# Optimization experiments

Hardware: AMD Instinct MI355X
Metric: run time of the kernel (lower is better)

Reference implementation:

```python
import jax, jax.numpy as jnp
import numpy as np

V, D, S, B, NL = 32000, 512, 1024, 2, 2
DS, KC, DI, DFF, E, TOPK = 16, 4, 1024, 2048, 8, 2
EPS = 1e-6


def rmsnorm(x, w):
    return x * jax.lax.rsqrt(jnp.mean(x * x, -1, keepdims=True) + EPS) * w


def mamba(x, in_w, conv_w, conv_b, x_proj_w, dt_w, dt_b, A_log, out_w):
    # x: (B, S, D)
    Bb, L, _ = x.shape
    xz = x @ in_w.T                      # (B, S, 2*DI)
    xi, z = jnp.split(xz, 2, axis=-1)    # each (B, S, DI)
    # causal depthwise conv (pad k-1 left == torch pad k-1 both + trim to L)
    xc = jnp.swapaxes(xi, 1, 2)          # (B, DI, S)
    xc = jax.lax.conv_general_dilated(
        xc, conv_w, window_strides=(1,), padding=[(KC - 1, 0)],
        dimension_numbers=("NCH", "OIH", "NCH"), feature_group_count=DI)
    xi = jnp.swapaxes(xc + conv_b[None, :, None], 1, 2)  # (B, S, DI)
    x_dbl = xi @ x_proj_w.T              # (B, S, 2*DS)
    B_param = x_dbl[..., DS:]            # (B, S, DS); first chunk overwritten in source
    delta = jax.nn.softplus(xi @ dt_w.T + dt_b)          # (B, S, DS)
    A = -jnp.exp(A_log)                  # (DI, DS)
    # recurrence coefficients (state dim summed out, as in source)
    a = jnp.exp(delta[:, :, None, :] * A[None, None]).sum(-1)        # (B, S, DI)
    b = xi * (delta * B_param).sum(-1, keepdims=True)                # (B, S, DI)

    def step(y, ab):
        at, bt = ab
        y = at * y + bt
        return y, y

    _, ys = jax.lax.scan(step, jnp.zeros((Bb, DI), x.dtype),
                         (jnp.swapaxes(a, 0, 1), jnp.swapaxes(b, 0, 1)))
    y = jnp.swapaxes(ys, 0, 1)           # (B, S, DI)
    y = y * jax.nn.silu(z)
    return y @ out_w.T                   # (B, S, D)


def moe(x, rw, rb, w1, b1, w2, b2):
    router_logits = x @ rw.T + rb                     # (B, S, E)
    probs = jax.nn.softmax(router_logits, axis=-1)
    topv, topi = jax.lax.top_k(probs, TOPK)
    wts = topv / topv.sum(-1, keepdims=True)          # renormalized gates
    h = jax.nn.gelu(jnp.einsum("bsd,efd->bsef", x, w1) + b1)   # (B, S, E, DFF)
    eo = jnp.einsum("bsef,edf->bsed", h, w2) + b2               # (B, S, E, D)
    sel = jnp.take_along_axis(eo, topi[..., None], axis=2)      # (B, S, K, D)
    out = (wts[..., None] * sel).sum(2)
    # load-balancing aux loss
    f = jax.nn.one_hot(topi, E).sum(2).mean((0, 1)) / TOPK
    P = probs.mean((0, 1))
    aux = E * jnp.sum(f * P)
    return out, aux


def setup_inputs() -> dict:
    key = jax.random.key(0)
    ks = jax.random.split(key, 16)
    f = lambda k, s: jax.random.normal(k, s, dtype=jnp.float32) * 0.02
    return {
        "input_ids": jax.random.randint(ks[0], (B, S), 0, V),
        "tok_emb": f(ks[1], (V, D)),
        "pos_emb": f(ks[2], (S, D)),
        "norm1_w": jnp.ones((NL, D), jnp.float32),
        "norm2_w": jnp.ones((NL, D), jnp.float32),
        "in_proj_w": f(ks[3], (NL, 2 * DI, D)),
        "conv_w": f(ks[4], (NL, DI, 1, KC)),
        "conv_b": jnp.zeros((NL, DI), jnp.float32),
        "x_proj_w": f(ks[5], (NL, 2 * DS, DI)),
        "dt_proj_w": f(ks[6], (NL, DS, DI)),
        "dt_proj_b": jnp.zeros((NL, DS), jnp.float32),
        "A_log": jnp.tile(jnp.log(jnp.arange(1, DS + 1, dtype=jnp.float32)), (NL, DI, 1)),
        "D_param": jnp.ones((NL, DI), jnp.float32),  # unused in forward, as in source
        "out_proj_w": f(ks[7], (NL, D, DI)),
        "router_w": f(ks[8], (NL, E, D)),
        "router_b": jnp.zeros((NL, E), jnp.float32),
        "w1": f(ks[9], (NL, E, DFF, D)),
        "b1": jnp.zeros((NL, E, DFF), jnp.float32),
        "w2": f(ks[10], (NL, E, D, DFF)),
        "b2": jnp.zeros((NL, E, D), jnp.float32),
        "final_norm_w": jnp.ones((D,), jnp.float32),
        "lm_head_w": f(ks[11], (V, D)),
    }


def reference(input_ids, tok_emb, pos_emb, norm1_w, norm2_w, in_proj_w, conv_w,
              conv_b, x_proj_w, dt_proj_w, dt_proj_b, A_log, D_param, out_proj_w,
              router_w, router_b, w1, b1, w2, b2, final_norm_w, lm_head_w):
    x = tok_emb[input_ids] + pos_emb[None, :, :]
    aux_total = jnp.zeros((), x.dtype)
    for l in range(NL):
        m = mamba(rmsnorm(x, norm1_w[l]), in_proj_w[l], conv_w[l], conv_b[l],
                  x_proj_w[l], dt_proj_w[l], dt_proj_b[l], A_log[l], out_proj_w[l])
        x = x + m
        ff, aux = moe(rmsnorm(x, norm2_w[l]), router_w[l], router_b[l],
                      w1[l], b1[l], w2[l], b2[l])
        x = x + ff
        aux_total = aux_total + aux
    x = rmsnorm(x, final_norm_w)
    logits = x @ lm_head_w.T
    return logits, aux_total
```

## Files before the change

kernel.cpp:

```cpp
#include <hip/hip_runtime.h>
#include <math.h>

#define S_    1024
#define D_    512
#define DI_   1024
#define DS_   16
#define KC_   4
#define E_    8
#define DFF_  2048
#define NTOK  2048
#define VOCAB 32000
#define NCHUNK 16
#define CHL    64
#define NSLOT 4096

typedef unsigned short ushort;
typedef unsigned int   uint;
typedef __attribute__((ext_vector_type(8))) short short8;
typedef __attribute__((ext_vector_type(4))) float f32x4;

#define IN_US   0ull
#define INL_US  1048576ull
#define OUT_US  2097152ull
#define OUTL_US 2621440ull
#define W1_US   3145728ull
#define W1L_US  11534336ull
#define W2_US   19922944ull
#define W2L_US  28311552ull
#define LAYER_US 36700160ull
#define LM_US   73400320ull
#define IN4   262144
#define OUT4  393216
#define W14   2490368
#define L4    4587520
#define LM4   4096000
#define LMEND 13271040
#define TOT4  13279232

__device__ __forceinline__ float gelu_sig(float x){
  float u = x*(1.5957691216057308f + 0.07135481627f*x*x);
  return x / (1.0f + expf(-u));
}
__device__ __forceinline__ ushort f2bf_rnd(float f){
  uint u = __float_as_uint(f);
  return (ushort)((u + 0x8000u) >> 16);
}
__device__ __forceinline__ float bf2f(ushort h){
  return __uint_as_float(((uint)h) << 16);
}
__device__ __forceinline__ void split1(float f, ushort& h, ushort& l){
  h = f2bf_rnd(f);
  float fh = bf2f(h);
  l = (ushort)(__float_as_uint(f - fh) >> 16);
}
__device__ __forceinline__ void gl16(void* lds, const void* g){
  __builtin_amdgcn_global_load_lds(
      (const __attribute__((address_space(1))) void*)g,
      (__attribute__((address_space(3))) void*)lds, 16, 0, 0);
}

__global__ __launch_bounds__(128) void k_embed(const int* __restrict__ ids,
    const float* __restrict__ tok, const float* __restrict__ pos, float* __restrict__ x){
  int t  = blockIdx.x;
  int d4 = threadIdx.x << 2;
  int s  = t & (S_-1);
  int id = ids[t];
  float4 tv = *(const float4*)(tok + (size_t)id*D_ + d4);
  float4 pv = *(const float4*)(pos + (size_t)s*D_ + d4);
  float4 o; o.x=tv.x+pv.x; o.y=tv.y+pv.y; o.z=tv.z+pv.z; o.w=tv.w+pv.w;
  *(float4*)(x + (size_t)t*D_ + d4) = o;
}

__global__ __launch_bounds__(256) void k_split_all(
    const float* __restrict__ in_w, const float* __restrict__ out_w,
    const float* __restrict__ w1, const float* __restrict__ w2,
    const float* __restrict__ lm, const float* __restrict__ Alog,
    ushort* __restrict__ wsp, float* __restrict__ negA){
  int g = blockIdx.x*256 + threadIdx.x;
  if (g >= TOT4) return;
  if (g < 2*L4){
    int l = (g < L4) ? 0 : 1;
    int r = g - l*L4;
    const float* src; size_t dh_off, dl_off;
    if (r < IN4){
      src = in_w + (size_t)l*1048576 + (size_t)r*4;
      dh_off = (size_t)l*LAYER_US + IN_US  + (size_t)r*4;
      dl_off = (size_t)l*LAYER_US + INL_US + (size_t)r*4;
    } else if (r < OUT4){
      int r2 = r - IN4;
      src = out_w + (size_t)l*524288 + (size_t)r2*4;
      dh_off = (size_t)l*LAYER_US + OUT_US  + (size_t)r2*4;
      dl_off = (size_t)l*LAYER_US + OUTL_US + (size_t)r2*4;
    } else if (r < W14){
      int r3 = r - OUT4;
      src = w1 + (size_t)l*8388608 + (size_t)r3*4;
      dh_off = (size_t)l*LAYER_US + W1_US  + (size_t)r3*4;
      dl_off = (size_t)l*LAYER_US + W1L_US + (size_t)r3*4;
    } else {
      int r4 = r - W14;
      src = w2 + (size_t)l*8388608 + (size_t)r4*4;
      dh_off = (size_t)l*LAYER_US + W2_US  + (size_t)r4*4;
      dl_off = (size_t)l*LAYER_US + W2L_US + (size_t)r4*4;
    }
    float4 v = *(const float4*)src;
    ushort h0,h1,h2,h3,l0,l1,l2,l3;
    split1(v.x,h0,l0); split1(v.y,h1,l1); split1(v.z,h2,l2); split1(v.w,h3,l3);
    *(uint2*)(wsp + dh_off) = make_uint2((uint)h0|((uint)h1<<16), (uint)h2|((uint)h3<<16));
    *(uint2*)(wsp + dl_off) = make_uint2((uint)l0|((uint)l1<<16), (uint)l2|((uint)l3<<16));
  } else if (g < LMEND){
    int r = g - 2*L4;
    float4 v = *(const float4*)(lm + (size_t)r*4);
    ushort h0 = f2bf_rnd(v.x), h1 = f2bf_rnd(v.y), h2 = f2bf_rnd(v.z), h3 = f2bf_rnd(v.w);
    *(uint2*)(wsp + LM_US + (size_t)r*4) = make_uint2((uint)h0|((uint)h1<<16), (uint)h2|((uint)h3<<16));
  } else {
    int r = g - LMEND;
    float4 v = *(const float4*)(Alog + (size_t)r*4);
    float4 o; o.x=-expf(v.x); o.y=-expf(v.y); o.z=-expf(v.z); o.w=-expf(v.w);
    *(float4*)(negA + (size_t)r*4) = o;
  }
}

template<int ADD>
__global__ __launch_bounds__(128) void k_rmsnorm_split(float* __restrict__ x,
    const float* __restrict__ P3, const int* __restrict__ slotmap,
    const float* __restrict__ w, ushort* __restrict__ oh, ushort* __restrict__ ol){
  int t = blockIdx.x;
  int d4 = threadIdx.x << 2;
  float4 v = *(const float4*)(x + (size_t)t*D_ + d4);
  if (ADD){
    int s0 = slotmap[2*t], s1 = slotmap[2*t+1];
    #pragma unroll
    for (int ks=0; ks<4; ++ks){
      float4 p0 = *(const float4*)(P3 + ((size_t)ks*NSLOT + s0)*D_ + d4);
      float4 p1 = *(const float4*)(P3 + ((size_t)ks*NSLOT + s1)*D_ + d4);
      v.x += p0.x + p1.x; v.y += p0.y + p1.y; v.z += p0.z + p1.z; v.w += p0.w + p1.w;
    }
    *(float4*)(x + (size_t)t*D_ + d4) = v;
  }
  float ss = v.x*v.x + v.y*v.y + v.z*v.z + v.w*v.w;
  #pragma unroll
  for (int off=32; off>=1; off>>=1) ss += __shfl_down(ss, off);
  __shared__ float sred[2];
  if ((threadIdx.x & 63) == 0) sred[threadIdx.x >> 6] = ss;
  __syncthreads();
  float total = sred[0] + sred[1];
  float scale = 1.0f / sqrtf(total * (1.0f/D_) + 1e-6f);
  float4 wv = *(const float4*)(w + d4);
  float4 o; o.x=v.x*scale*wv.x; o.y=v.y*scale*wv.y; o.z=v.z*scale*wv.z; o.w=v.w*scale*wv.w;
  ushort h0,h1,h2,h3,l0,l1,l2,l3;
  split1(o.x,h0,l0); split1(o.y,h1,l1); split1(o.z,h2,l2); split1(o.w,h3,l3);
  *(uint2*)(oh + (size_t)t*D_ + d4) = make_uint2((uint)h0|((uint)h1<<16), (uint)h2|((uint)h3<<16));
  *(uint2*)(ol + (size_t)t*D_ + d4) = make_uint2((uint)l0|((uint)l1<<16), (uint)l2|((uint)l3<<16));
}

__global__ __launch_bounds__(128) void k_rmsnorm_router(float* __restrict__ x,
    const float* __restrict__ P2, const float* __restrict__ w,
    const float* __restrict__ rw, const float* __restrict__ rb,
    ushort* __restrict__ oh, ushort* __restrict__ ol,
    float* __restrict__ probs, float* __restrict__ topw, int* __restrict__ topi){
  int t = blockIdx.x;
  int tid = threadIdx.x;
  int d4 = tid << 2;
  float4 v = *(const float4*)(x + (size_t)t*D_ + d4);
  #pragma unroll
  for (int ks=0; ks<4; ++ks){
    float4 p = *(const float4*)(P2 + (size_t)ks*NTOK*D_ + (size_t)t*D_ + d4);
    v.x += p.x; v.y += p.y; v.z += p.z; v.w += p.w;
  }
  *(float4*)(x + (size_t)t*D_ + d4) = v;
  float ss = v.x*v.x + v.y*v.y + v.z*v.z + v.w*v.w;
  #pragma unroll
  for (int off=32; off>=1; off>>=1) ss += __shfl_down(ss, off);
  __shared__ float sred[2];
  __shared__ float lg2[2][E_];
  __shared__ float lg[E_];
  if ((tid & 63) == 0) sred[tid >> 6] = ss;
  __syncthreads();
  float total = sred[0] + sred[1];
  float scale = 1.0f / sqrtf(total * (1.0f/D_) + 1e-6f);
  float4 wv = *(const float4*)(w + d4);
  float4 o; o.x=v.x*scale*wv.x; o.y=v.y*scale*wv.y; o.z=v.z*scale*wv.z; o.w=v.w*scale*wv.w;
  ushort h0,h1,h2,h3,l0,l1,l2,l3;
  split1(o.x,h0,l0); split1(o.y,h1,l1); split1(o.z,h2,l2); split1(o.w,h3,l3);
  *(uint2*)(oh + (size_t)t*D_ + d4) = make_uint2((uint)h0|((uint)h1<<16), (uint)h2|((uint)h3<<16));
  *(uint2*)(ol + (size_t)t*D_ + d4) = make_uint2((uint)l0|((uint)l1<<16), (uint)l2|((uint)l3<<16));
  int lane = tid & 63, wid2 = tid >> 6;
  #pragma unroll
  for (int e=0;e<E_;e++){
    const float* rr = rw + (size_t)e*D_ + d4;
    float p = o.x*rr[0] + o.y*rr[1] + o.z*rr[2] + o.w*rr[3];
    #pragma unroll
    for (int off=32; off>=1; off>>=1) p += __shfl_down(p, off);
    if (lane==0) lg2[wid2][e] = p;
  }
  __syncthreads();
  if (tid==0){
    #pragma unroll
    for (int e=0;e<E_;e++) lg[e] = lg2[0][e] + lg2[1][e] + rb[e];
    float mx = lg[0];
    #pragma unroll
    for (int e=1;e<E_;e++) mx = fmaxf(mx, lg[e]);
    float pe[E_]; float sum = 0.f;
    #pragma unroll
    for (int e=0;e<E_;e++){ pe[e] = expf(lg[e]-mx); sum += pe[e]; }
    #pragma unroll
    for (int e=0;e<E_;e++){ pe[e] /= sum; probs[(size_t)t*E_ + e] = pe[e]; }
    int i1 = 0;
    #pragma unroll
    for (int e=1;e<E_;e++) if (pe[e] > pe[i1]) i1 = e;
    int i2 = (i1==0) ? 1 : 0;
    #pragma unroll
    for (int e=0;e<E_;e++) if (e!=i1 && pe[e] > pe[i2]) i2 = e;
    float wsum = pe[i1] + pe[i2];
    topw[t*2]   = pe[i1]/wsum;
    topw[t*2+1] = pe[i2]/wsum;
    topi[t*2] = i1; topi[t*2+1] = i2;
  }
}

template<int EPI, int NT, int KSP>
__global__ __launch_bounds__(256, 4) void gemm_mfma(
    const ushort* __restrict__ Ahg, const ushort* __restrict__ Alg,
    const ushort* __restrict__ Whb, const ushort* __restrict__ Wlb,
    float* __restrict__ Cb, ushort* __restrict__ Chh, ushort* __restrict__ Chl,
    const float* __restrict__ biasb, const float* __restrict__ slotw,
    const int* __restrict__ gidx, const int* __restrict__ offs,
    int M, int N, int K)
{
  int e, ksp;
  if (KSP > 1){ e = blockIdx.z / KSP; ksp = blockIdx.z % KSP; }
  else        { e = blockIdx.z;       ksp = 0; }
  int off = 0, cnt = M;
  if (EPI==1 || EPI==3){
    off = offs[e];
    cnt = offs[e+1] - off;
    if ((int)(blockIdx.x*128) >= cnt) return;
  }
  const size_t wbase = (size_t)((EPI==1||EPI==3) ? e : 0) * N * K;
  const ushort* Whg = Whb + wbase;
  const ushort* Wlg = Wlb + wbase;
  const float* bias = (EPI==1||EPI==3) ? (biasb + (size_t)e * N) : biasb;

  __shared__ ushort sAh[128*32];
  __shared__ ushort sWh[128*32];
  __shared__ ushort sAl[(NT>1)?(128*32):8];
  __shared__ ushort sWl[(NT>1)?(128*32):8];

  const int tid  = threadIdx.x;
  const int row0 = blockIdx.x * 128;
  const int col0 = blockIdx.y * 128;
  const int lane = tid & 63;
  const int wid  = tid >> 6;

  const int srow0  = wid*32 + (lane>>2);
  const int srow1  = srow0 + 16;
  const int schunk = (lane&3) ^ ((lane>>2)&3);
  const int ldsb0  = (wid*32)      * 32;
  const int ldsb1  = (wid*32 + 16) * 32;

  const int k0 = ksp * (K / KSP);
  const int nk = K / KSP;

  int ar0, ar1;
  if (EPI==1){
    int l0i = row0 + srow0; if (l0i > cnt-1) l0i = cnt-1;
    int l1i = row0 + srow1; if (l1i > cnt-1) l1i = cnt-1;
    ar0 = gidx[off + l0i]; ar1 = gidx[off + l1i];
  } else if (EPI==3){
    int l0i = row0 + srow0; if (l0i > cnt-1) l0i = cnt-1;
    int l1i = row0 + srow1; if (l1i > cnt-1) l1i = cnt-1;
    ar0 = off + l0i; ar1 = off + l1i;
  } else {
    ar0 = row0 + srow0; ar1 = row0 + srow1;
  }
  const ushort* gah0 = Ahg + (size_t)ar0*K + k0 + schunk*8;
  const ushort* gah1 = Ahg + (size_t)ar1*K + k0 + schunk*8;
  const ushort* gwh0 = Whg + (size_t)(col0 + srow0)*K + k0 + schunk*8;
  const ushort* gwh1 = Whg + (size_t)(col0 + srow1)*K + k0 + schunk*8;
  const ushort* gal0 = nullptr; const ushort* gal1 = nullptr;
  const ushort* gwl0 = nullptr; const ushort* gwl1 = nullptr;
  if (NT>1){
    gal0 = Alg + (size_t)ar0*K + k0 + schunk*8;
    gal1 = Alg + (size_t)ar1*K + k0 + schunk*8;
    gwl0 = Wlg + (size_t)(col0 + srow0)*K + k0 + schunk*8;
    gwl1 = Wlg + (size_t)(col0 + srow1)*K + k0 + schunk*8;
  }

  const int lr  = lane & 15;
  const int kq  = lane >> 4;
  const int kx  = ((kq ^ (lr & 3)) << 3);
  const int wrM = (wid >> 1) * 64;
  const int wcN = (wid & 1) * 64;

  f32x4 zero = {0.f, 0.f, 0.f, 0.f};
  f32x4 acc[4][4];
  #pragma unroll
  for (int i=0;i<4;i++)
    #pragma unroll
    for (int j=0;j<4;j++) acc[i][j] = zero;

  for (int kk=0; kk<nk; kk+=32){
    __syncthreads();
    gl16(&sAh[ldsb0], gah0 + kk);
    gl16(&sAh[ldsb1], gah1 + kk);
    gl16(&sWh[ldsb0], gwh0 + kk);
    gl16(&sWh[ldsb1], gwh1 + kk);
    if (NT>1){
      gl16(&sAl[ldsb0], gal0 + kk);
      gl16(&sAl[ldsb1], gal1 + kk);
      gl16(&sWl[ldsb0], gwl0 + kk);
      gl16(&sWl[ldsb1], gwl1 + kk);
    }
    __syncthreads();

    short8 fah[4], fal[4], fbh[4], fbl[4];
    #pragma unroll
    for (int f=0; f<4; ++f){
      int rA = wrM + f*16 + lr;
      int rB = wcN + f*16 + lr;
      fah[f] = *(const short8*)&sAh[rA*32 + kx];
      fbh[f] = *(const short8*)&sWh[rB*32 + kx];
      if (NT>1){
        fal[f] = *(const short8*)&sAl[rA*32 + kx];
        fbl[f] = *(const short8*)&sWl[rB*32 + kx];
      }
    }
    #pragma unroll
    for (int i=0;i<4;i++)
      #pragma unroll
      for (int j=0;j<4;j++){
        f32x4 c = acc[i][j];
        if (NT==4) c = __builtin_amdgcn_mfma_f32_16x16x32_bf16(fal[i], fbl[j], c, 0,0,0);
        if (NT>1){
          c = __builtin_amdgcn_mfma_f32_16x16x32_bf16(fal[i], fbh[j], c, 0,0,0);
          c = __builtin_amdgcn_mfma_f32_16x16x32_bf16(fah[i], fbl[j], c, 0,0,0);
        }
        c = __builtin_amdgcn_mfma_f32_16x16x32_bf16(fah[i], fbh[j], c, 0,0,0);
        acc[i][j] = c;
      }
  }

  float bj[4];
  if (EPI==1 || EPI==3){
    #pragma unroll
    for (int j=0;j<4;j++) bj[j] = bias[col0 + wcN + j*16 + lr];
  }
  #pragma unroll
  for (int i=0;i<4;i++){
    #pragma unroll
    for (int jj=0;jj<4;jj++){
      int rt   = wrM + i*16 + kq*4 + jj;
      int grow = row0 + rt;
      if (EPI==0){
        float* cr = Cb + (size_t)grow*N + col0 + wcN + lr;
        #pragma unroll
        for (int j=0;j<4;j++) cr[j*16] = acc[i][j][jj];
      } else if (EPI==2){
        float* cr = Cb + (size_t)ksp*M*N + (size_t)grow*N + col0 + wcN + lr;
        #pragma unroll
        for (int j=0;j<4;j++) cr[j*16] = acc[i][j][jj];
      } else if (EPI==1){
        if (grow < cnt){
          int slot = off + grow;
          size_t base = (size_t)slot*N + col0 + wcN + lr;
          #pragma unroll
          for (int j=0;j<4;j++){
            float g = gelu_sig(acc[i][j][jj] + bj[j]);
            ushort hh, ll; split1(g, hh, ll);
            Chh[base + j*16] = hh; Chl[base + j*16] = ll;
          }
        }
      } else {
        if (grow < cnt){
          int slot = off + grow;
          float sw = slotw[slot];
          float* cr = Cb + ((size_t)ksp*NSLOT + slot)*N + col0 + wcN + lr;
          #pragma unroll
          for (int j=0;j<4;j++){
            float v = acc[i][j][jj];
            if (ksp==0) v += bj[j];
            cr[j*16] = sw*v;
          }
        }
      }
    }
  }
}

__global__ __launch_bounds__(256) void k_convab(const float* __restrict__ xz,
    const float* __restrict__ cw, const float* __restrict__ cb,
    const float* __restrict__ xpw, const float* __restrict__ dtw,
    const float* __restrict__ dtb, const float* __restrict__ negA,
    float* __restrict__ a, float* __restrict__ bb){
  int t = blockIdx.x;
  int b = t >> 10, s = t & (S_-1);
  int tid = threadIdx.x;
  int c0 = tid << 2;
  __shared__ float xrow[DI_];
  __shared__ float outv[32];
  __shared__ float dl[DS_+1];
  float4 acc = *(const float4*)(cb + c0);
  #pragma unroll
  for (int k=0;k<KC_;k++){
    int ss = s - (KC_-1) + k;
    if (ss >= 0){
      float4 xv = *(const float4*)(xz + ((size_t)(b*S_+ss))*(2*DI_) + c0);
      acc.x += xv.x * cw[(c0+0)*KC_ + k];
      acc.y += xv.y * cw[(c0+1)*KC_ + k];
      acc.z += xv.z * cw[(c0+2)*KC_ + k];
      acc.w += xv.w * cw[(c0+3)*KC_ + k];
    }
  }
  *(float4*)(xrow + c0) = acc;
  __syncthreads();
  int wid = tid >> 6, lane = tid & 63;
  #pragma unroll
  for (int oi=0; oi<8; ++oi){
    int o = wid*8 + oi;
    const float* wr = (o < 16) ? (xpw + (size_t)(DS_ + o)*DI_) : (dtw + (size_t)(o-16)*DI_);
    float sum = 0.f;
    #pragma unroll
    for (int j=0;j<16;j++) sum += xrow[lane + 64*j] * wr[lane + 64*j];
    #pragma unroll
    for (int off=32; off>=1; off>>=1) sum += __shfl_down(sum, off);
    if (lane == 0) outv[o] = sum;
  }
  __syncthreads();
  if (tid < DS_){
    float d  = outv[16+tid] + dtb[tid];
    float sp = fmaxf(d, 0.f) + log1pf(expf(-fabsf(d)));
    dl[tid] = sp;
    float pr = sp * outv[tid];
    #pragma unroll
    for (int off=8; off>=1; off>>=1) pr += __shfl_down(pr, off);
    if (tid == 0) dl[DS_] = pr;
  }
  __syncthreads();
  float sdbv = dl[DS_];
  float av[4];
  #pragma unroll
  for (int i=0;i<4;i++){
    const float* nA = negA + (size_t)(c0+i)*DS_;
    float sum = 0.f;
    #pragma unroll
    for (int ds=0; ds<DS_; ds++) sum += expf(dl[ds] * nA[ds]);
    av[i] = sum;
  }
  *(float4*)(a + (size_t)t*DI_ + c0) = make_float4(av[0],av[1],av[2],av[3]);
  float4 bv; bv.x=acc.x*sdbv; bv.y=acc.y*sdbv; bv.z=acc.z*sdbv; bv.w=acc.w*sdbv;
  *(float4*)(bb + (size_t)t*DI_ + c0) = bv;
}

__global__ __launch_bounds__(256) void k_scan1(const float* __restrict__ a,
    const float* __restrict__ bb, float* __restrict__ aprod, float* __restrict__ yend){
  int g  = blockIdx.x*256 + threadIdx.x;
  int di = g & (DI_-1);
  int c  = (g >> 10) & (NCHUNK-1);
  int b  = g >> 14;
  float ap = 1.f, y = 0.f;
  size_t base = ((size_t)b*S_ + (size_t)c*CHL)*DI_ + di;
  #pragma unroll 4
  for (int i=0;i<CHL;i++){
    float at = a[base + (size_t)i*DI_], bt = bb[base + (size_t)i*DI_];
    y = at*y + bt; ap *= at;
  }
  aprod[g] = ap; yend[g] = y;
}

__global__ __launch_bounds__(256) void k_scan2(const float* __restrict__ a,
    const float* __restrict__ bb, const float* __restrict__ xz,
    const float* __restrict__ aprod, const float* __restrict__ yend,
    ushort* __restrict__ yh, ushort* __restrict__ yl){
  int g  = blockIdx.x*256 + threadIdx.x;
  int di = g & (DI_-1);
  int c  = (g >> 10) & (NCHUNK-1);
  int b  = g >> 14;
  float y = 0.f;
  for (int j=0;j<c;j++){
    int gg = ((b*NCHUNK + j) << 10) + di;
    y = aprod[gg]*y + yend[gg];
  }
  size_t base = ((size_t)b*S_ + (size_t)c*CHL)*DI_ + di;
  #pragma unroll 4
  for (int i=0;i<CHL;i++){
    float at = a[base + (size_t)i*DI_], bt = bb[base + (size_t)i*DI_];
    y = at*y + bt;
    float z = xz[((size_t)(b*S_ + c*CHL + i))*(2*DI_) + DI_ + di];
    float sil = z / (1.f + expf(-z));
    float v = y * sil;
    ushort hh, ll; split1(v, hh, ll);
    yh[base + (size_t)i*DI_] = hh;
    yl[base + (size_t)i*DI_] = ll;
  }
}

__global__ __launch_bounds__(512) void k_compact_aux(const int* __restrict__ topi,
    const float* __restrict__ topw, const float* __restrict__ probs,
    int* __restrict__ gidx, float* __restrict__ asgw, int* __restrict__ slotmap,
    int* __restrict__ offs, float* __restrict__ dst, int first){
  int tid = threadIdx.x;
  int e = tid >> 6, lane = tid & 63;
  __shared__ unsigned char stop[NTOK*2];
  __shared__ float stw[NTOK*2];
  __shared__ int counts[E_];
  __shared__ float red[8][E_];
  for (int i = tid; i < NTOK*2; i += 512){
    stop[i] = (unsigned char)topi[i];
    stw[i]  = topw[i];
  }
  float ps[E_];
  #pragma unroll
  for (int q=0;q<E_;q++) ps[q]=0.f;
  for (int t = tid; t < NTOK; t += 512){
    float4 p0 = *(const float4*)(probs + (size_t)t*E_);
    float4 p1 = *(const float4*)(probs + (size_t)t*E_ + 4);
    ps[0]+=p0.x; ps[1]+=p0.y; ps[2]+=p0.z; ps[3]+=p0.w;
    ps[4]+=p1.x; ps[5]+=p1.y; ps[6]+=p1.z; ps[7]+=p1.w;
  }
  #pragma unroll
  for (int q=0;q<E_;q++){
    float v = ps[q];
    #pragma unroll
    for (int off=32; off>=1; off>>=1) v += __shfl_down(v, off);
    if (lane==0) red[e][q] = v;
  }
  __syncthreads();
  int cnt = 0;
  for (int c=0; c<NTOK/64; ++c){
    int t = c*64 + lane;
    bool flag = (stop[2*t]==e) || (stop[2*t+1]==e);
    unsigned long long m = __ballot(flag);
    cnt += __popcll(m);
  }
  if (lane==0) counts[e] = cnt;
  __syncthreads();
  int base = 0;
  for (int i=0;i<e;i++) base += counts[i];
  if (lane==0) offs[e] = base;
  if (tid==0){
    int tot=0;
    for (int i=0;i<E_;i++) tot += counts[i];
    offs[E_] = tot;
  }
  int run = base;
  for (int c=0; c<NTOK/64; ++c){
    int t = c*64 + lane;
    int which = (stop[2*t]==e) ? 0 : ((stop[2*t+1]==e) ? 1 : -1);
    bool flag = which >= 0;
    unsigned long long m = __ballot(flag);
    int rank = __popcll(m & ((1ull<<lane)-1ull));
    if (flag){
      int pos = run + rank;
      gidx[pos] = t;
      asgw[pos] = stw[2*t+which];
      slotmap[2*t+which] = pos;
    }
    run += __popcll(m);
  }
  if (tid==0){
    float aux = 0.f;
    #pragma unroll
    for (int i=0;i<E_;i++){
      float P = 0.f;
      #pragma unroll
      for (int wdd=0; wdd<8; ++wdd) P += red[wdd][i];
      P *= (1.0f/NTOK);
      float f = (float)counts[i] * (1.0f/(NTOK*2.0f));
      aux += f*P;
    }
    aux *= (float)E_;
    if (first) dst[0] = aux; else dst[0] += aux;
  }
}

extern "C" void kernel_launch(void* const* d_in, const int* in_sizes, int n_in,
                              void* d_out, int out_size, void* d_ws, size_t ws_size,
                              hipStream_t stream) {
  const int*   input_ids  = (const int*)  d_in[0];
  const float* tok_emb    = (const float*)d_in[1];
  const float* pos_emb    = (const float*)d_in[2];
  const float* norm1_w    = (const float*)d_in[3];
  const float* norm2_w    = (const float*)d_in[4];
  const float* in_proj_w  = (const float*)d_in[5];
  const float* conv_w     = (const float*)d_in[6];
  const float* conv_b     = (const float*)d_in[7];
  const float* x_proj_w   = (const float*)d_in[8];
  const float* dt_proj_w  = (const float*)d_in[9];
  const float* dt_proj_b  = (const float*)d_in[10];
  const float* A_log      = (const float*)d_in[11];
  const float* out_proj_w = (const float*)d_in[13];
  const float* router_w   = (const float*)d_in[14];
  const float* router_b   = (const float*)d_in[15];
  const float* w1         = (const float*)d_in[16];
  const float* b1         = (const float*)d_in[17];
  const float* w2         = (const float*)d_in[18];
  const float* b2         = (const float*)d_in[19];
  const float* final_norm = (const float*)d_in[20];
  const float* lm_head_w  = (const float*)d_in[21];
  float* out = (float*)d_out;

  float* f0 = (float*)d_ws;
  float*  x    = f0;
  ushort* xnh  = (ushort*)(f0 + 1048576);
  ushort* xnl  = xnh + 1048576;
  float*  xz   = f0 + 2097152;
  float*  a    = f0 + 6291456;
  float*  bb   = f0 + 8388608;
  ushort* yh   = (ushort*)(f0 + 10485760);
  ushort* yl   = yh + 2097152;
  ushort* hh   = (ushort*)(f0 + 12582912);
  ushort* hl   = hh + 8388608;
  float*  P2   = f0 + 20971520;
  float*  P3   = f0 + 25165824;
  ushort* wsplit = (ushort*)(f0 + 33554432);
  float*  negA = f0 + 78446592;
  float*  aprod= negA + 32768;
  float*  yendb= aprod + 32768;
  float*  probs= yendb + 32768;
  float*  topw = probs + 16384;
  float*  asgw = topw + 4096;
  int*    topi = (int*)(asgw + 4096);
  int*    gidx = topi + 4096;
  int*    slotmap = gidx + 4096;
  int*    offs = slotmap + 4096;

  float* aux_dst = out + (size_t)NTOK*VOCAB;

  k_split_all<<<(TOT4+255)/256, 256, 0, stream>>>(in_proj_w, out_proj_w, w1, w2,
                                                  lm_head_w, A_log, wsplit, negA);
  k_embed<<<NTOK, 128, 0, stream>>>(input_ids, tok_emb, pos_emb, x);

  for (int l=0; l<2; ++l){
    ushort* L = wsplit + (size_t)l*LAYER_US;
    if (l == 0)
      k_rmsnorm_split<0><<<NTOK, 128, 0, stream>>>(x, nullptr, nullptr,
          norm1_w + (size_t)l*D_, xnh, xnl);
    else
      k_rmsnorm_split<1><<<NTOK, 128, 0, stream>>>(x, P3, slotmap,
          norm1_w + (size_t)l*D_, xnh, xnl);
    gemm_mfma<0,3,1><<<dim3(16,16,1), 256, 0, stream>>>(xnh, xnl, L+IN_US, L+INL_US,
        xz, nullptr, nullptr, nullptr, nullptr, nullptr, nullptr, NTOK, 2*DI_, D_);
    k_convab<<<NTOK, 256, 0, stream>>>(xz, conv_w + (size_t)l*DI_*KC_, conv_b + (size_t)l*DI_,
                                       x_proj_w + (size_t)l*2*DS_*DI_,
                                       dt_proj_w + (size_t)l*DS_*DI_, dt_proj_b + (size_t)l*DS_,
                                       negA + (size_t)l*DI_*DS_, a, bb);
    k_scan1<<<(NTOK*NCHUNK)/256, 256, 0, stream>>>(a, bb, aprod, yendb);
    k_scan2<<<(NTOK*NCHUNK)/256, 256, 0, stream>>>(a, bb, xz, aprod, yendb, yh, yl);
    gemm_mfma<2,3,4><<<dim3(16,4,4), 256, 0, stream>>>(yh, yl, L+OUT_US, L+OUTL_US,
        P2, nullptr, nullptr, nullptr, nullptr, nullptr, nullptr, NTOK, D_, DI_);
    k_rmsnorm_router<<<NTOK, 128, 0, stream>>>(x, P2, norm2_w + (size_t)l*D_,
        router_w + (size_t)l*E_*D_, router_b + (size_t)l*E_,
        xnh, xnl, probs, topw, topi);
    k_compact_aux<<<1, 512, 0, stream>>>(topi, topw, probs, gidx, asgw, slotmap, offs,
                                         aux_dst, l==0 ? 1 : 0);
    gemm_mfma<1,3,1><<<dim3(16,16,8), 256, 0, stream>>>(xnh, xnl, L+W1_US, L+W1L_US,
        nullptr, hh, hl, b1 + (size_t)l*E_*DFF_, nullptr, gidx, offs, 0, DFF_, D_);
    gemm_mfma<3,3,4><<<dim3(16,4,32), 256, 0, stream>>>(hh, hl, L+W2_US, L+W2L_US,
        P3, nullptr, nullptr, b2 + (size_t)l*E_*D_, asgw, gidx, offs, 0, D_, DFF_);
  }

  k_rmsnorm_split<1><<<NTOK, 128, 0, stream>>>(x, P3, slotmap, final_norm, xnh, xnl);
  gemm_mfma<0,1,1><<<dim3(16,250,1), 256, 0, stream>>>(xnh, nullptr, wsplit + LM_US, nullptr,
      out, nullptr, nullptr, nullptr, nullptr, nullptr, nullptr, NTOK, VOCAB, D_);
}
```

Baseline: 932.1 us.

## Drop lo-split terms for layer-1 MoE GEMMs, add wider LM-head GEMM, reswizzle LDS

The second layer's MoE expert GEMMs now run a single bf16 pass instead of the three-term hi/lo split, and the weight-split kernel skips writing low halves for those weights. The LDS swizzle pattern changes to use different lane bits, and the LM head gets a dedicated 128x256-tile GEMM kernel with launch bounds allowing two blocks per SM. The intent is to cut MFMA work and memory traffic on the largest GEMMs and reduce LDS bank conflicts. The cost is lower precision in layer-1 MoE outputs, which may affect accuracy tolerance, and higher register pressure in the new LM kernel.

```diff
diff --git a/kernel.cpp b/kernel.cpp
--- a/kernel.cpp
+++ b/kernel.cpp
@@ -82,6 +82,7 @@
     int l = (g < L4) ? 0 : 1;
     int r = g - l*L4;
     const float* src; size_t dh_off, dl_off;
+    bool wlo = true;
     if (r < IN4){
       src = in_w + (size_t)l*1048576 + (size_t)r*4;
       dh_off = (size_t)l*LAYER_US + IN_US  + (size_t)r*4;
@@ -96,17 +97,20 @@
       src = w1 + (size_t)l*8388608 + (size_t)r3*4;
       dh_off = (size_t)l*LAYER_US + W1_US  + (size_t)r3*4;
       dl_off = (size_t)l*LAYER_US + W1L_US + (size_t)r3*4;
+      wlo = (l == 0);
     } else {
       int r4 = r - W14;
       src = w2 + (size_t)l*8388608 + (size_t)r4*4;
       dh_off = (size_t)l*LAYER_US + W2_US  + (size_t)r4*4;
       dl_off = (size_t)l*LAYER_US + W2L_US + (size_t)r4*4;
+      wlo = (l == 0);
     }
     float4 v = *(const float4*)src;
     ushort h0,h1,h2,h3,l0,l1,l2,l3;
     split1(v.x,h0,l0); split1(v.y,h1,l1); split1(v.z,h2,l2); split1(v.w,h3,l3);
     *(uint2*)(wsp + dh_off) = make_uint2((uint)h0|((uint)h1<<16), (uint)h2|((uint)h3<<16));
-    *(uint2*)(wsp + dl_off) = make_uint2((uint)l0|((uint)l1<<16), (uint)l2|((uint)l3<<16));
+    if (wlo)
+      *(uint2*)(wsp + dl_off) = make_uint2((uint)l0|((uint)l1<<16), (uint)l2|((uint)l3<<16));
   } else if (g < LMEND){
     int r = g - 2*L4;
     float4 v = *(const float4*)(lm + (size_t)r*4);
@@ -254,7 +258,7 @@
 
   const int srow0  = wid*32 + (lane>>2);
   const int srow1  = srow0 + 16;
-  const int schunk = (lane&3) ^ ((lane>>2)&3);
+  const int schunk = (lane&3) ^ ((lane>>3)&3);
   const int ldsb0  = (wid*32)      * 32;
   const int ldsb1  = (wid*32 + 16) * 32;
 
@@ -288,7 +292,7 @@
 
   const int lr  = lane & 15;
   const int kq  = lane >> 4;
-  const int kx  = ((kq ^ (lr & 3)) << 3);
+  const int kx  = ((kq ^ ((lr>>1)&3)) << 3);
   const int wrM = (wid >> 1) * 64;
   const int wcN = (wid & 1) * 64;
 
@@ -366,8 +370,12 @@
           #pragma unroll
           for (int j=0;j<4;j++){
             float g = gelu_sig(acc[i][j][jj] + bj[j]);
-            ushort hh, ll; split1(g, hh, ll);
-            Chh[base + j*16] = hh; Chl[base + j*16] = ll;
+            ushort hh_ = f2bf_rnd(g);
+            Chh[base + j*16] = hh_;
+            if (NT>1){
+              ushort ll_ = (ushort)(__float_as_uint(g - bf2f(hh_)) >> 16);
+              Chl[base + j*16] = ll_;
+            }
           }
         }
       } else {
@@ -383,6 +391,82 @@
           }
         }
       }
+    }
+  }
+}
+
+__global__ __launch_bounds__(256, 2) void gemm_lm(
+    const ushort* __restrict__ Ahg, const ushort* __restrict__ Whg,
+    float* __restrict__ Cb, int M, int N, int K)
+{
+  __shared__ ushort sAh[128*32];
+  __shared__ ushort sWh[256*32];
+  const int tid  = threadIdx.x;
+  const int row0 = blockIdx.x * 128;
+  const int col0 = blockIdx.y * 256;
+  const int lane = tid & 63;
+  const int wid  = tid >> 6;
+
+  const int schunk = (lane&3) ^ ((lane>>3)&3);
+  const int srowA  = wid*32 + (lane>>2);
+  const int ldsA0  = (wid*32)*32;
+  const int ldsA1  = (wid*32+16)*32;
+  const ushort* ga0 = Ahg + (size_t)(row0 + srowA)*K + schunk*8;
+  const ushort* ga1 = Ahg + (size_t)(row0 + srowA + 16)*K + schunk*8;
+
+  const int srowW  = wid*64 + (lane>>2);
+  const int ldsW0  = (wid*64)*32,    ldsW1 = (wid*64+16)*32;
+  const int ldsW2  = (wid*64+32)*32, ldsW3 = (wid*64+48)*32;
+  const ushort* gw0 = Whg + (size_t)(col0 + srowW)*K      + schunk*8;
+  const ushort* gw1 = Whg + (size_t)(col0 + srowW + 16)*K + schunk*8;
+  const ushort* gw2 = Whg + (size_t)(col0 + srowW + 32)*K + schunk*8;
+  const ushort* gw3 = Whg + (size_t)(col0 + srowW + 48)*K + schunk*8;
+
+  const int lr  = lane & 15;
+  const int kq  = lane >> 4;
+  const int kx  = ((kq ^ ((lr>>1)&3)) << 3);
+  const int wrM = (wid >> 1) * 64;
+  const int wcN = (wid & 1) * 128;
+
+  f32x4 zero = {0.f, 0.f, 0.f, 0.f};
+  f32x4 acc[4][8];
+  #pragma unroll
+  for (int i=0;i<4;i++)
+    #pragma unroll
+    for (int j=0;j<8;j++) acc[i][j] = zero;
+
+  for (int kk=0; kk<K; kk+=32){
+    __syncthreads();
+    gl16(&sAh[ldsA0], ga0 + kk);
+    gl16(&sAh[ldsA1], ga1 + kk);
+    gl16(&sWh[ldsW0], gw0 + kk);
+    gl16(&sWh[ldsW1], gw1 + kk);
+    gl16(&sWh[ldsW2], gw2 + kk);
+    gl16(&sWh[ldsW3], gw3 + kk);
+    __syncthreads();
+
+    short8 fa[4], fb[8];
+    #pragma unroll
+    for (int f=0; f<4; ++f)
+      fa[f] = *(const short8*)&sAh[(wrM + f*16 + lr)*32 + kx];
+    #pragma unroll
+    for (int f=0; f<8; ++f)
+      fb[f] = *(const short8*)&sWh[(wcN + f*16 + lr)*32 + kx];
+    #pragma unroll
+    for (int i=0;i<4;i++)
+      #pragma unroll
+      for (int j=0;j<8;j++)
+        acc[i][j] = __builtin_amdgcn_mfma_f32_16x16x32_bf16(fa[i], fb[j], acc[i][j], 0,0,0);
+  }
+
+  #pragma unroll
+  for (int i=0;i<4;i++){
+    #pragma unroll
+    for (int jj=0;jj<4;jj++){
+      int grow = row0 + wrM + i*16 + kq*4 + jj;
+      float* cr = Cb + (size_t)grow*N + col0 + wcN + lr;
+      #pragma unroll
+      for (int j=0;j<8;j++) cr[j*16] = acc[i][j][jj];
     }
   }
 }
@@ -653,13 +737,19 @@
         xnh, xnl, probs, topw, topi);
     k_compact_aux<<<1, 512, 0, stream>>>(topi, topw, probs, gidx, asgw, slotmap, offs,
                                          aux_dst, l==0 ? 1 : 0);
-    gemm_mfma<1,3,1><<<dim3(16,16,8), 256, 0, stream>>>(xnh, xnl, L+W1_US, L+W1L_US,
-        nullptr, hh, hl, b1 + (size_t)l*E_*DFF_, nullptr, gidx, offs, 0, DFF_, D_);
-    gemm_mfma<3,3,4><<<dim3(16,4,32), 256, 0, stream>>>(hh, hl, L+W2_US, L+W2L_US,
-        P3, nullptr, nullptr, b2 + (size_t)l*E_*D_, asgw, gidx, offs, 0, D_, DFF_);
+    if (l == 0){
+      gemm_mfma<1,3,1><<<dim3(16,16,8), 256, 0, stream>>>(xnh, xnl, L+W1_US, L+W1L_US,
+          nullptr, hh, hl, b1 + (size_t)l*E_*DFF_, nullptr, gidx, offs, 0, DFF_, D_);
+      gemm_mfma<3,3,4><<<dim3(16,4,32), 256, 0, stream>>>(hh, hl, L+W2_US, L+W2L_US,
+          P3, nullptr, nullptr, b2 + (size_t)l*E_*D_, asgw, gidx, offs, 0, D_, DFF_);
+    } else {
+      gemm_mfma<1,1,1><<<dim3(16,16,8), 256, 0, stream>>>(xnh, nullptr, L+W1_US, nullptr,
+          nullptr, hh, nullptr, b1 + (size_t)l*E_*DFF_, nullptr, gidx, offs, 0, DFF_, D_);
+      gemm_mfma<3,1,4><<<dim3(16,4,32), 256, 0, stream>>>(hh, nullptr, L+W2_US, nullptr,
+          P3, nullptr, nullptr, b2 + (size_t)l*E_*D_, asgw, gidx, offs, 0, D_, DFF_);
+    }
   }
 
   k_rmsnorm_split<1><<<NTOK, 128, 0, stream>>>(x, P3, slotmap, final_norm, xnh, xnl);
-  gemm_mfma<0,1,1><<<dim3(16,250,1), 256, 0, stream>>>(xnh, nullptr, wsplit + LM_US, nullptr,
-      out, nullptr, nullptr, nullptr, nullptr, nullptr, nullptr, NTOK, VOCAB, D_);
-}
+  gemm_lm<<<dim3(16,125,1), 256, 0, stream>>>(xnh, wsplit + LM_US, out, NTOK, VOCAB, D_);
+}
```

After: 831.9 us. 1.12x faster.
